# Kernel tuning notes

Hardware: AMD Instinct MI355X
Metric: run time of the kernel (lower is better)

Reference implementation:

```python
import jax, jax.numpy as jnp
import numpy as np

B, Q, D, H, CTX, W_OUT = 2048, 256, 64, 128, 5, 32


def setup_inputs() -> dict:
    key = jax.random.key(0)
    ks = jax.random.split(key, 20)
    s = 0.05
    p = lambda k, shape: jax.random.normal(k, shape, dtype=jnp.float32) * s
    return {
        "x_in": jax.random.normal(ks[0], (B, Q, D), dtype=jnp.float32),
        "w_out": W_OUT,
        "conv_w": p(ks[1], (H, 3 * D, CTX)),
        "conv_b": p(ks[2], (H,)),
        "fc1_w": p(ks[3], (H, H)),
        "fc1_b": p(ks[4], (H,)),
        "fc2_w": p(ks[5], (D, H)),
        "fc2_b": p(ks[6], (D,)),
        "rot1_w": p(ks[7], (H, D)),
        "rot1_b": p(ks[8], (H,)),
        "rot2_w": p(ks[9], (2, H)),
        "rot2_b": p(ks[10], (2,)),
        "gru_wih": p(ks[11], (3 * H, D)),
        "gru_whh": p(ks[12], (3 * H, H)),
        "gru_bih": p(ks[13], (3 * H,)),
        "gru_bhh": p(ks[14], (3 * H,)),
        "out_w": p(ks[15], (D, H)),
        "out_b": p(ks[16], (D,)),
    }


def reference(x_in, w_out, conv_w, conv_b, fc1_w, fc1_b, fc2_w, fc2_b,
              rot1_w, rot1_b, rot2_w, rot2_b, gru_wih, gru_whh,
              gru_bih, gru_bhh, out_w, out_b):
    b, q, d = x_in.shape
    h_dim = fc1_w.shape[0]
    ctx = conv_w.shape[2]
    m = d // 2
    pi = np.float32(np.pi)

    def kalman_step(carry, y_t):
        x_post, y_prev, buf = carry
        # rotation params from posterior state
        rp = jnp.maximum(x_post @ rot1_w.T + rot1_b, 0.0) @ rot2_w.T + rot2_b
        rho = jax.nn.sigmoid(rp[:, 0:1]) * 1.5
        phi = jnp.tanh(rp[:, 1:2]) * pi
        # complex polar rotation: (a+ib) * rho*e^{i phi}
        a, bb = x_post[:, :m], x_post[:, m:]
        c = rho * jnp.cos(phi)
        s = rho * jnp.sin(phi)
        x_pri = jnp.concatenate([a * c - bb * s, a * s + bb * c], axis=1)
        innov = y_t - x_pri
        diff = y_t - y_prev
        feat = jnp.concatenate([innov, x_post, diff], axis=1)  # (B, 3D)
        # roll context buffer, append newest features
        buf = jnp.concatenate([buf[:, :, 1:], feat[:, :, None]], axis=2)
        # Conv1d(kernel=context, pad=0) over a context-length buffer == full contraction
        t = jnp.einsum('hck,bck->bh', conv_w, buf) + conv_b
        t = jnp.maximum(t, 0.0)
        t = jnp.maximum(t @ fc1_w.T + fc1_b, 0.0)
        K = jax.nn.sigmoid(t @ fc2_w.T + fc2_b)  # (B, D)
        x_post_new = x_pri + K * innov
        return (x_post_new, y_t, buf), None

    init = (jnp.zeros((b, d), x_in.dtype),
            x_in[:, 0, :],
            jnp.zeros((b, 3 * d, ctx), x_in.dtype))
    (x_post, _, _), _ = jax.lax.scan(kalman_step, init, jnp.swapaxes(x_in, 0, 1))

    def gru_step(carry, _):
        h, curr = carry
        gi = curr @ gru_wih.T + gru_bih
        gh = h @ gru_whh.T + gru_bhh
        i_r, i_z, i_n = jnp.split(gi, 3, axis=1)
        h_r, h_z, h_n = jnp.split(gh, 3, axis=1)
        r = jax.nn.sigmoid(i_r + h_r)
        z = jax.nn.sigmoid(i_z + h_z)
        n = jnp.tanh(i_n + r * h_n)
        h_new = (1.0 - z) * n + z * h
        curr_new = curr + (h_new @ out_w.T + out_b)
        return (h_new, curr_new), curr_new

    (_, _), preds = jax.lax.scan(
        gru_step, (jnp.zeros((b, h_dim), x_in.dtype), x_post), None, length=w_out)
    return jnp.swapaxes(preds, 0, 1)  # (B, w_out, D)
```

## Files before the change

kernel.cpp:

```cpp
#include <hip/hip_runtime.h>

#define QLEN 256
#define DDIM 64
#define WOUT 32

typedef __bf16 b8v __attribute__((ext_vector_type(8)));
typedef float f4v __attribute__((ext_vector_type(4)));

__device__ __forceinline__ f4v MFMA(b8v a, b8v b, f4v c) {
  return __builtin_amdgcn_mfma_f32_16x16x32_bf16(a, b, c, 0, 0, 0);
}
__device__ __forceinline__ float sigmoidf_(float x) { return 1.0f/(1.0f+__expf(-x)); }
__device__ __forceinline__ float tanhf_(float x)    { return 1.0f - 2.0f/(__expf(2.0f*x)+1.0f); }
__device__ __forceinline__ b8v lda(const __bf16* p, const __bf16* zp, bool pr) {
  return *(const b8v*)(pr ? p : zp);
}

__global__ __launch_bounds__(512, 2)
void k_kalman(const float* __restrict__ x_in,
              const float* __restrict__ conv_w, const float* __restrict__ conv_b,
              const float* __restrict__ fc1_w,  const float* __restrict__ fc1_b,
              const float* __restrict__ fc2_w,  const float* __restrict__ fc2_b,
              const float* __restrict__ rot1_w, const float* __restrict__ rot1_b,
              const float* __restrict__ rot2_w, const float* __restrict__ rot2_b,
              float* __restrict__ out)
{
  __shared__ __align__(16) __bf16 SMB[11872];
  __shared__ __align__(16) float  SMF[1536];
  const int tid = threadIdx.x;
  const int w  = tid >> 6;
  const int l  = tid & 63;
  const int lr = l & 15;
  const int lg = l >> 4;
  const int wg = blockIdx.x;
  const bool pr8 = (lr < 8);

  __bf16* XPB  = SMB;
  __bf16* T1   = SMB + 576;
  __bf16* TC   = SMB + 1664;
  __bf16* T2   = SMB + 2752;
  __bf16* FEAT = SMB + 3840;
  const __bf16* ZP = SMB + 11840;
  float*  XPF  = SMF;
  float*  XPRI = SMF + 512;
  float*  INV  = SMF + 1024;

  for (int i = tid; i < 11872; i += 512) SMB[i] = (__bf16)0.0f;
  for (int i = tid; i < 1536;  i += 512) SMF[i] = 0.0f;

  const int hcol = 16*w + lr;

  b8v r1B[2], f1B[4], f2B[4], cvB[30];
  #pragma unroll
  for (int q = 0; q < 2; ++q)
    #pragma unroll
    for (int j = 0; j < 8; ++j)
      r1B[q][j] = (__bf16)rot1_w[hcol*64 + q*32 + lg*8 + j];
  #pragma unroll
  for (int q = 0; q < 4; ++q)
    #pragma unroll
    for (int j = 0; j < 8; ++j)
      f1B[q][j] = (__bf16)fc1_w[hcol*128 + q*32 + lg*8 + j];
  {
    const int h2 = (w < 4) ? hcol : 0;
    #pragma unroll
    for (int q = 0; q < 4; ++q)
      #pragma unroll
      for (int j = 0; j < 8; ++j)
        f2B[q][j] = (__bf16)fc2_w[h2*128 + q*32 + lg*8 + j];
  }
  #pragma unroll
  for (int c = 0; c < 30; ++c) {
    const int L = c/6, q = c%6;
    #pragma unroll
    for (int j = 0; j < 8; ++j)
      cvB[c][j] = (__bf16)conv_w[hcol*960 + (q*32 + lg*8 + j)*5 + (4-L)];
  }

  const float b_r1 = rot1_b[hcol];
  const float b_f1 = fc1_b[hcol];
  const float b_f2 = fc2_b[(w < 4) ? hcol : 0];
  const float bc   = conv_b[hcol];
  const float r2w00 = rot2_w[l],       r2w01 = rot2_w[64 + l];
  const float r2w10 = rot2_w[128 + l], r2w11 = rot2_w[192 + l];
  const float rb0 = rot2_b[0], rb1 = rot2_b[1];
  const float PI_F = 3.14159274f;

  const float* xptr = x_in + ((long)(wg*8 + w)*QLEN)*DDIM + l;
  float y_cur = xptr[0];
  float y_prv = y_cur;
  int slot = 0;

  __syncthreads();

  for (int t = 0; t < QLEN; ++t) {
    {
      b8v a0 = lda(&XPB[lr*72      + lg*8], ZP, pr8);
      b8v a1 = lda(&XPB[lr*72 + 32 + lg*8], ZP, pr8);
      f4v C = {};
      C = MFMA(a0, r1B[0], C);
      C = MFMA(a1, r1B[1], C);
      if (lg < 2) {
        #pragma unroll
        for (int r = 0; r < 4; ++r) {
          float v = C[r] + b_r1; v = v > 0.f ? v : 0.f;
          T1[(lg*4+r)*136 + hcol] = (__bf16)v;
        }
      }
    }
    __syncthreads();

    float y_nxt = (t+1 < QLEN) ? xptr[(t+1)*DDIM] : y_cur;
    f4v Ca = {}, Cb = {};
    {
      const __bf16* fb1 = FEAT + ((slot-1+5)%5)*1600 + lr*200 + lg*8;
      const __bf16* fb2 = FEAT + ((slot-2+5)%5)*1600 + lr*200 + lg*8;
      const __bf16* fb3 = FEAT + ((slot-3+5)%5)*1600 + lr*200 + lg*8;
      const __bf16* fb4 = FEAT + ((slot-4+5)%5)*1600 + lr*200 + lg*8;
      #pragma unroll
      for (int c = 6; c < 30; ++c) {
        const int L = c/6, q = c%6;
        const __bf16* fb = (L==1) ? fb1 : (L==2) ? fb2 : (L==3) ? fb3 : fb4;
        b8v a = lda(&fb[q*32], ZP, pr8);
        if (c & 1) Cb = MFMA(a, cvB[c], Cb); else Ca = MFMA(a, cvB[c], Ca);
      }
    }
    {
      float t1a = (float)T1[w*136 + l];
      float t1b = (float)T1[w*136 + 64 + l];
      float acc0 = t1a*r2w00 + t1b*r2w01;
      float acc1 = t1a*r2w10 + t1b*r2w11;
      #pragma unroll
      for (int m = 1; m < 64; m <<= 1) {
        acc0 += __shfl_xor(acc0, m, 64);
        acc1 += __shfl_xor(acc1, m, 64);
      }
      float rho = 1.5f * sigmoidf_(acc0 + rb0);
      float phi = PI_F * tanhf_(acc1 + rb1);
      float cc = rho * __cosf(phi);
      float ss = rho * __sinf(phi);
      float lo32 = XPF[w*64 + (l & 31)];
      float hi32 = XPF[w*64 + (l & 31) + 32];
      float xpri = (l < 32) ? (lo32*cc - hi32*ss) : (lo32*ss + hi32*cc);
      float innov = y_cur - xpri;
      float diff  = y_cur - y_prv;
      __bf16* fr = FEAT + slot*1600 + w*200;
      fr[l]       = (__bf16)innov;
      fr[128 + l] = (__bf16)diff;
      XPRI[w*64 + l] = xpri;
      INV [w*64 + l] = innov;
    }
    __syncthreads();

    {
      const __bf16* fb0 = FEAT + slot*1600 + lr*200 + lg*8;
      #pragma unroll
      for (int c = 0; c < 6; ++c) {
        b8v a = lda(&fb0[c*32], ZP, pr8);
        if (c & 1) Cb = MFMA(a, cvB[c], Cb); else Ca = MFMA(a, cvB[c], Ca);
      }
      if (lg < 2) {
        #pragma unroll
        for (int r = 0; r < 4; ++r) {
          float v = Ca[r] + Cb[r] + bc; v = v > 0.f ? v : 0.f;
          TC[(lg*4+r)*136 + hcol] = (__bf16)v;
        }
      }
    }
    __syncthreads();

    {
      f4v D0 = {}, D1 = {};
      #pragma unroll
      for (int q = 0; q < 4; ++q) {
        b8v a = lda(&TC[lr*136 + q*32 + lg*8], ZP, pr8);
        if (q & 1) D1 = MFMA(a, f1B[q], D1); else D0 = MFMA(a, f1B[q], D0);
      }
      if (lg < 2) {
        #pragma unroll
        for (int r = 0; r < 4; ++r) {
          float v = D0[r] + D1[r] + b_f1; v = v > 0.f ? v : 0.f;
          T2[(lg*4+r)*136 + hcol] = (__bf16)v;
        }
      }
    }
    __syncthreads();

    const int slot_next = (slot == 4) ? 0 : slot + 1;
    if (w < 4) {
      f4v D0 = {}, D1 = {};
      #pragma unroll
      for (int q = 0; q < 4; ++q) {
        b8v a = lda(&T2[lr*136 + q*32 + lg*8], ZP, pr8);
        if (q & 1) D1 = MFMA(a, f2B[q], D1); else D0 = MFMA(a, f2B[q], D0);
      }
      if (lg < 2) {
        #pragma unroll
        for (int r = 0; r < 4; ++r) {
          int e = lg*4 + r;
          float K = sigmoidf_(D0[r] + D1[r] + b_f2);
          float xn = XPRI[e*64 + hcol] + K * INV[e*64 + hcol];
          XPF[e*64 + hcol] = xn;
          XPB[e*72 + hcol] = (__bf16)xn;
          FEAT[slot_next*1600 + e*200 + 64 + hcol] = (__bf16)xn;
        }
      }
    }
    __syncthreads();

    y_prv = y_cur; y_cur = y_nxt;
    slot = slot_next;
  }

  out[((long)(wg*8 + w)*WOUT)*DDIM + l] = XPF[w*64 + l];
}

__global__ __launch_bounds__(512, 2)
void k_gru(const float* __restrict__ gru_wih, const float* __restrict__ gru_whh,
           const float* __restrict__ gru_bih, const float* __restrict__ gru_bhh,
           const float* __restrict__ out_w,   const float* __restrict__ out_b,
           float* __restrict__ out)
{
  __shared__ __align__(16) __bf16 CUR[16*72];
  __shared__ __align__(16) __bf16 HB [16*136];
  const int tid = threadIdx.x;
  const int w  = tid >> 6, l = tid & 63, lr = l & 15, lg = l >> 4;
  const int g = blockIdx.x;

  for (int i = tid; i < 16*136; i += 512) HB[i] = (__bf16)0.f;
  for (int i = tid; i < 16*72; i += 512) CUR[i] = (__bf16)0.f;
  __syncthreads();
  for (int i = tid; i < 8*64; i += 512) {
    int e = i >> 6, d = i & 63;
    CUR[e*72 + d] = (__bf16)out[((long)(g*8 + e)*WOUT)*DDIM + d];
  }

  b8v fih[3][2], fhh[3][4], fo[4];
  #pragma unroll
  for (int n3 = 0; n3 < 3; ++n3) {
    int row = 16*(w + 8*n3) + lr;
    #pragma unroll
    for (int q = 0; q < 2; ++q)
      #pragma unroll
      for (int j = 0; j < 8; ++j)
        fih[n3][q][j] = (__bf16)gru_wih[row*64 + q*32 + lg*8 + j];
    #pragma unroll
    for (int q = 0; q < 4; ++q)
      #pragma unroll
      for (int j = 0; j < 8; ++j)
        fhh[n3][q][j] = (__bf16)gru_whh[row*128 + q*32 + lg*8 + j];
  }
  {
    int row = 16*(w & 3) + lr;
    #pragma unroll
    for (int q = 0; q < 4; ++q)
      #pragma unroll
      for (int j = 0; j < 8; ++j)
        fo[q][j] = (__bf16)out_w[row*128 + q*32 + lg*8 + j];
  }
  const int jh = 16*w + lr;
  const float b_ir = gru_bih[jh], b_iz = gru_bih[128+jh], b_in = gru_bih[256+jh];
  const float b_hr = gru_bhh[jh], b_hz = gru_bhh[128+jh], b_hn = gru_bhh[256+jh];
  const float b_o  = out_b[16*(w & 3) + lr];
  const int dcol = 16*(w & 3) + lr;
  __syncthreads();

  for (int s = 0; s < WOUT; ++s) {
    f4v cI[3] = {}, cH[3] = {};
    #pragma unroll
    for (int q = 0; q < 2; ++q) {
      b8v a = *(const b8v*)&CUR[lr*72 + q*32 + lg*8];
      #pragma unroll
      for (int n3 = 0; n3 < 3; ++n3) cI[n3] = MFMA(a, fih[n3][q], cI[n3]);
    }
    #pragma unroll
    for (int q = 0; q < 4; ++q) {
      b8v a = *(const b8v*)&HB[lr*136 + q*32 + lg*8];
      #pragma unroll
      for (int n3 = 0; n3 < 3; ++n3) cH[n3] = MFMA(a, fhh[n3][q], cH[n3]);
    }
    __syncthreads();

    #pragma unroll
    for (int r = 0; r < 4; ++r) {
      int e = lg*4 + r;
      float ir = cI[0][r] + b_ir, iz = cI[1][r] + b_iz, in_ = cI[2][r] + b_in;
      float hr = cH[0][r] + b_hr, hz = cH[1][r] + b_hz, hn  = cH[2][r] + b_hn;
      float rr = sigmoidf_(ir + hr);
      float zz = sigmoidf_(iz + hz);
      float nn = tanhf_(in_ + rr*hn);
      float hold = (float)HB[e*136 + jh];
      float hnew = (1.f - zz)*nn + zz*hold;
      HB[e*136 + jh] = (__bf16)hnew;
    }
    __syncthreads();

    if (w < 4) {
      f4v C0 = {};
      #pragma unroll
      for (int q = 0; q < 4; ++q) {
        b8v a = *(const b8v*)&HB[lr*136 + q*32 + lg*8];
        C0 = MFMA(a, fo[q], C0);
      }
      #pragma unroll
      for (int r = 0; r < 4; ++r) {
        int e = lg*4 + r;
        float cn = (float)CUR[e*72 + dcol] + C0[r] + b_o;
        CUR[e*72 + dcol] = (__bf16)cn;
        if (e < 8)
          out[(((long)(g*8 + e))*WOUT + s)*DDIM + dcol] = cn;
      }
    }
    __syncthreads();
  }
}

extern "C" void kernel_launch(void* const* d_in, const int* in_sizes, int n_in,
                              void* d_out, int out_size, void* d_ws, size_t ws_size,
                              hipStream_t stream) {
  (void)in_sizes; (void)n_in; (void)d_ws; (void)ws_size; (void)out_size;
  const float* x_in   = (const float*)d_in[0];
  const float* conv_w = (const float*)d_in[2];
  const float* conv_b = (const float*)d_in[3];
  const float* fc1_w  = (const float*)d_in[4];
  const float* fc1_b  = (const float*)d_in[5];
  const float* fc2_w  = (const float*)d_in[6];
  const float* fc2_b  = (const float*)d_in[7];
  const float* rot1_w = (const float*)d_in[8];
  const float* rot1_b = (const float*)d_in[9];
  const float* rot2_w = (const float*)d_in[10];
  const float* rot2_b = (const float*)d_in[11];
  const float* gwih   = (const float*)d_in[12];
  const float* gwhh   = (const float*)d_in[13];
  const float* gbih   = (const float*)d_in[14];
  const float* gbhh   = (const float*)d_in[15];
  const float* ow     = (const float*)d_in[16];
  const float* ob     = (const float*)d_in[17];
  float* out = (float*)d_out;

  k_kalman<<<256, 512, 0, stream>>>(x_in, conv_w, conv_b, fc1_w, fc1_b,
                                    fc2_w, fc2_b, rot1_w, rot1_b,
                                    rot2_w, rot2_b, out);
  k_gru<<<256, 512, 0, stream>>>(gwih, gwhh, gbih, gbhh, ow, ob, out);
}
```

Measured before the change: 692.6 us.

## Split conv contraction across wave pairs with LDS partial-sum reduction

Each wave now computes two conv output tiles over half of the 30 K-chunks instead of one tile over all 30. Waves 0-3 and 4-7 split the chunks and reduce their partial sums through a new shared buffer, which costs one extra barrier per step. The current-step chunks are ordered last in the split, so less work waits behind the feature-write barrier. Per-lane shared-memory pointers are hoisted out of the loop in place of per-load select logic, and three accumulator pairs give more independent MFMA chains.

```diff
diff --git a/kernel.cpp b/kernel.cpp
--- a/kernel.cpp
+++ b/kernel.cpp
@@ -12,9 +12,6 @@
 }
 __device__ __forceinline__ float sigmoidf_(float x) { return 1.0f/(1.0f+__expf(-x)); }
 __device__ __forceinline__ float tanhf_(float x)    { return 1.0f - 2.0f/(__expf(2.0f*x)+1.0f); }
-__device__ __forceinline__ b8v lda(const __bf16* p, const __bf16* zp, bool pr) {
-  return *(const b8v*)(pr ? p : zp);
-}
 
 __global__ __launch_bounds__(512, 2)
 void k_kalman(const float* __restrict__ x_in,
@@ -25,14 +22,15 @@
               const float* __restrict__ rot2_w, const float* __restrict__ rot2_b,
               float* __restrict__ out)
 {
-  __shared__ __align__(16) __bf16 SMB[11872];
-  __shared__ __align__(16) float  SMF[1536];
+  __shared__ __align__(16) __bf16 SMB[12064];
+  __shared__ __align__(16) float  SMF[3584];
   const int tid = threadIdx.x;
   const int w  = tid >> 6;
   const int l  = tid & 63;
   const int lr = l & 15;
   const int lg = l >> 4;
   const int wg = blockIdx.x;
+  const bool lo  = (w < 4);
   const bool pr8 = (lr < 8);
 
   __bf16* XPB  = SMB;
@@ -40,17 +38,22 @@
   __bf16* TC   = SMB + 1664;
   __bf16* T2   = SMB + 2752;
   __bf16* FEAT = SMB + 3840;
-  const __bf16* ZP = SMB + 11840;
+  __bf16* ZROW = SMB + 11856;
   float*  XPF  = SMF;
   float*  XPRI = SMF + 512;
   float*  INV  = SMF + 1024;
-
-  for (int i = tid; i < 11872; i += 512) SMB[i] = (__bf16)0.0f;
-  for (int i = tid; i < 1536;  i += 512) SMF[i] = 0.0f;
+  float*  PART = SMF + 1536;
+
+  for (int i = tid; i < 12064; i += 512) SMB[i] = (__bf16)0.0f;
+  for (int i = tid; i < 3584;  i += 512) SMF[i] = 0.0f;
 
   const int hcol = 16*w + lr;
-
-  b8v r1B[2], f1B[4], f2B[4], cvB[30];
+  const int t0   = 2*(w & 3);
+
+  constexpr int CH_LO[15] = {2, 6,7,8, 12,13,14, 18,19,20, 24,25,26, 0,1};
+  constexpr int CH_HI[15] = {3, 9,10,11, 15,16,17, 21,22,23, 27,28,29, 4,5};
+
+  b8v r1B[2], f1B[4], f2B[4], cvB[15][2];
   #pragma unroll
   for (int q = 0; q < 2; ++q)
     #pragma unroll
@@ -62,7 +65,7 @@
     for (int j = 0; j < 8; ++j)
       f1B[q][j] = (__bf16)fc1_w[hcol*128 + q*32 + lg*8 + j];
   {
-    const int h2 = (w < 4) ? hcol : 0;
+    const int h2 = lo ? hcol : 0;
     #pragma unroll
     for (int q = 0; q < 4; ++q)
       #pragma unroll
@@ -70,22 +73,33 @@
         f2B[q][j] = (__bf16)fc2_w[h2*128 + q*32 + lg*8 + j];
   }
   #pragma unroll
-  for (int c = 0; c < 30; ++c) {
+  for (int i = 0; i < 15; ++i) {
+    const int c = lo ? CH_LO[i] : CH_HI[i];
     const int L = c/6, q = c%6;
     #pragma unroll
-    for (int j = 0; j < 8; ++j)
-      cvB[c][j] = (__bf16)conv_w[hcol*960 + (q*32 + lg*8 + j)*5 + (4-L)];
+    for (int ti = 0; ti < 2; ++ti)
+      #pragma unroll
+      for (int j = 0; j < 8; ++j)
+        cvB[i][ti][j] =
+          (__bf16)conv_w[((t0+ti)*16 + lr)*960 + (q*32 + lg*8 + j)*5 + (4-L)];
   }
 
   const float b_r1 = rot1_b[hcol];
   const float b_f1 = fc1_b[hcol];
-  const float b_f2 = fc2_b[(w < 4) ? hcol : 0];
-  const float bc   = conv_b[hcol];
+  const float b_f2 = fc2_b[lo ? hcol : 0];
+  const float bc0  = conv_b[t0*16 + lr];
+  const float bc1  = conv_b[(t0+1)*16 + lr];
   const float r2w00 = rot2_w[l],       r2w01 = rot2_w[64 + l];
   const float r2w10 = rot2_w[128 + l], r2w11 = rot2_w[192 + l];
   const float rb0 = rot2_b[0], rb1 = rot2_b[1];
   const float PI_F = 3.14159274f;
 
+  const __bf16* zb    = ZROW + lg*8;
+  const __bf16* xpb_p = pr8 ? (XPB + lr*72  + lg*8) : zb;
+  const __bf16* tc_p  = pr8 ? (TC  + lr*136 + lg*8) : zb;
+  const __bf16* t2_p  = pr8 ? (T2  + lr*136 + lg*8) : zb;
+  const __bf16* featb = FEAT + lr*200 + lg*8;
+
   const float* xptr = x_in + ((long)(wg*8 + w)*QLEN)*DDIM + l;
   float y_cur = xptr[0];
   float y_prv = y_cur;
@@ -95,8 +109,8 @@
 
   for (int t = 0; t < QLEN; ++t) {
     {
-      b8v a0 = lda(&XPB[lr*72      + lg*8], ZP, pr8);
-      b8v a1 = lda(&XPB[lr*72 + 32 + lg*8], ZP, pr8);
+      b8v a0 = *(const b8v*)(xpb_p);
+      b8v a1 = *(const b8v*)(xpb_p + 32);
       f4v C = {};
       C = MFMA(a0, r1B[0], C);
       C = MFMA(a1, r1B[1], C);
@@ -111,18 +125,23 @@
     __syncthreads();
 
     float y_nxt = (t+1 < QLEN) ? xptr[(t+1)*DDIM] : y_cur;
-    f4v Ca = {}, Cb = {};
-    {
-      const __bf16* fb1 = FEAT + ((slot-1+5)%5)*1600 + lr*200 + lg*8;
-      const __bf16* fb2 = FEAT + ((slot-2+5)%5)*1600 + lr*200 + lg*8;
-      const __bf16* fb3 = FEAT + ((slot-3+5)%5)*1600 + lr*200 + lg*8;
-      const __bf16* fb4 = FEAT + ((slot-4+5)%5)*1600 + lr*200 + lg*8;
-      #pragma unroll
-      for (int c = 6; c < 30; ++c) {
+    const __bf16* fbp[5];
+    #pragma unroll
+    for (int L = 0; L < 5; ++L) {
+      int s5 = slot - L; if (s5 < 0) s5 += 5;
+      fbp[L] = pr8 ? (featb + s5*1600) : zb;
+    }
+    f4v P0 = {}, P1 = {}, P2 = {}, Q0 = {}, Q1 = {}, Q2 = {};
+    {
+      #pragma unroll
+      for (int i = 0; i < 13; ++i) {
+        const int c = lo ? CH_LO[i] : CH_HI[i];
         const int L = c/6, q = c%6;
-        const __bf16* fb = (L==1) ? fb1 : (L==2) ? fb2 : (L==3) ? fb3 : fb4;
-        b8v a = lda(&fb[q*32], ZP, pr8);
-        if (c & 1) Cb = MFMA(a, cvB[c], Cb); else Ca = MFMA(a, cvB[c], Ca);
+        b8v a = *(const b8v*)&fbp[L][q*32];
+        const int s3 = i % 3;
+        if      (s3 == 0) { P0 = MFMA(a, cvB[i][0], P0); Q0 = MFMA(a, cvB[i][1], Q0); }
+        else if (s3 == 1) { P1 = MFMA(a, cvB[i][0], P1); Q1 = MFMA(a, cvB[i][1], Q1); }
+        else              { P2 = MFMA(a, cvB[i][0], P2); Q2 = MFMA(a, cvB[i][1], Q2); }
       }
     }
     {
@@ -153,17 +172,34 @@
     __syncthreads();
 
     {
-      const __bf16* fb0 = FEAT + slot*1600 + lr*200 + lg*8;
-      #pragma unroll
-      for (int c = 0; c < 6; ++c) {
-        b8v a = lda(&fb0[c*32], ZP, pr8);
-        if (c & 1) Cb = MFMA(a, cvB[c], Cb); else Ca = MFMA(a, cvB[c], Ca);
-      }
+      const __bf16* fb0 = pr8 ? (featb + slot*1600) : zb;
+      #pragma unroll
+      for (int i = 13; i < 15; ++i) {
+        const int q = (lo ? CH_LO[i] : CH_HI[i]) % 6;
+        b8v a = *(const b8v*)&fb0[q*32];
+        if (i == 13) { P0 = MFMA(a, cvB[i][0], P0); Q0 = MFMA(a, cvB[i][1], Q0); }
+        else         { P1 = MFMA(a, cvB[i][0], P1); Q1 = MFMA(a, cvB[i][1], Q1); }
+      }
+      if (!lo) {
+        f4v s0, s1;
+        #pragma unroll
+        for (int r = 0; r < 4; ++r) { s0[r] = P0[r]+P1[r]+P2[r]; s1[r] = Q0[r]+Q1[r]+Q2[r]; }
+        *(f4v*)&PART[(t0*16 + lr)*16 + lg*4]     = s0;
+        *(f4v*)&PART[((t0+1)*16 + lr)*16 + lg*4] = s1;
+      }
+    }
+    __syncthreads();
+
+    if (lo) {
+      f4v p0 = *(const f4v*)&PART[(t0*16 + lr)*16 + lg*4];
+      f4v p1 = *(const f4v*)&PART[((t0+1)*16 + lr)*16 + lg*4];
       if (lg < 2) {
         #pragma unroll
         for (int r = 0; r < 4; ++r) {
-          float v = Ca[r] + Cb[r] + bc; v = v > 0.f ? v : 0.f;
-          TC[(lg*4+r)*136 + hcol] = (__bf16)v;
+          float v0 = P0[r]+P1[r]+P2[r] + p0[r] + bc0; v0 = v0 > 0.f ? v0 : 0.f;
+          float v1 = Q0[r]+Q1[r]+Q2[r] + p1[r] + bc1; v1 = v1 > 0.f ? v1 : 0.f;
+          TC[(lg*4+r)*136 + t0*16 + lr]     = (__bf16)v0;
+          TC[(lg*4+r)*136 + (t0+1)*16 + lr] = (__bf16)v1;
         }
       }
     }
@@ -173,7 +209,7 @@
       f4v D0 = {}, D1 = {};
       #pragma unroll
       for (int q = 0; q < 4; ++q) {
-        b8v a = lda(&TC[lr*136 + q*32 + lg*8], ZP, pr8);
+        b8v a = *(const b8v*)(tc_p + q*32);
         if (q & 1) D1 = MFMA(a, f1B[q], D1); else D0 = MFMA(a, f1B[q], D0);
       }
       if (lg < 2) {
@@ -187,11 +223,11 @@
     __syncthreads();
 
     const int slot_next = (slot == 4) ? 0 : slot + 1;
-    if (w < 4) {
+    if (lo) {
       f4v D0 = {}, D1 = {};
       #pragma unroll
       for (int q = 0; q < 4; ++q) {
-        b8v a = lda(&T2[lr*136 + q*32 + lg*8], ZP, pr8);
+        b8v a = *(const b8v*)(t2_p + q*32);
         if (q & 1) D1 = MFMA(a, f2B[q], D1); else D0 = MFMA(a, f2B[q], D0);
       }
       if (lg < 2) {
```

New measurement: 1.374 ms. 98.3% more time.

## Carry conv partial sums across steps and parallelize rotation reduction

Applied to the files above, without the earlier changes.

Each feature frame's contribution to the conv is now accumulated once and carried forward in registers (U/V accumulators), so each step issues its conv MFMAs as soon as a frame is available. The history-frame MFMAs are spread over phases that were otherwise idle (alongside fc1 and fc2), taking them off the critical path. The rotation-head reduction now uses 16-lane shuffles plus a small shared partial-sum table instead of a bf16 T1 round-trip followed by a full 64-lane reduction. The predicated loads that fell back to a zero pad are dropped, and the layout of rows 8-15 relies on zero-initialized shared memory. The cost is more accumulator registers and a tighter dependency on that zero padding.

```diff
diff --git a/kernel.cpp b/kernel.cpp
--- a/kernel.cpp
+++ b/kernel.cpp
@@ -12,9 +12,6 @@
 }
 __device__ __forceinline__ float sigmoidf_(float x) { return 1.0f/(1.0f+__expf(-x)); }
 __device__ __forceinline__ float tanhf_(float x)    { return 1.0f - 2.0f/(__expf(2.0f*x)+1.0f); }
-__device__ __forceinline__ b8v lda(const __bf16* p, const __bf16* zp, bool pr) {
-  return *(const b8v*)(pr ? p : zp);
-}
 
 __global__ __launch_bounds__(512, 2)
 void k_kalman(const float* __restrict__ x_in,
@@ -25,28 +22,26 @@
               const float* __restrict__ rot2_w, const float* __restrict__ rot2_b,
               float* __restrict__ out)
 {
-  __shared__ __align__(16) __bf16 SMB[11872];
-  __shared__ __align__(16) float  SMF[1536];
+  __shared__ __align__(16) __bf16 SMB[12352];
+  __shared__ __align__(16) float  SMF[1792];
   const int tid = threadIdx.x;
   const int w  = tid >> 6;
   const int l  = tid & 63;
   const int lr = l & 15;
   const int lg = l >> 4;
   const int wg = blockIdx.x;
-  const bool pr8 = (lr < 8);
 
   __bf16* XPB  = SMB;
-  __bf16* T1   = SMB + 576;
-  __bf16* TC   = SMB + 1664;
-  __bf16* T2   = SMB + 2752;
-  __bf16* FEAT = SMB + 3840;
-  const __bf16* ZP = SMB + 11840;
+  __bf16* TC   = SMB + 576;
+  __bf16* T2   = SMB + 1664;
+  __bf16* FEAT = SMB + 2752;
   float*  XPF  = SMF;
   float*  XPRI = SMF + 512;
   float*  INV  = SMF + 1024;
-
-  for (int i = tid; i < 11872; i += 512) SMB[i] = (__bf16)0.0f;
-  for (int i = tid; i < 1536;  i += 512) SMF[i] = 0.0f;
+  float*  PR   = SMF + 1536;
+
+  for (int i = tid; i < 12352; i += 512) SMB[i] = (__bf16)0.0f;
+  for (int i = tid; i < 1792;  i += 512) SMF[i] = 0.0f;
 
   const int hcol = 16*w + lr;
 
@@ -81,8 +76,8 @@
   const float b_f1 = fc1_b[hcol];
   const float b_f2 = fc2_b[(w < 4) ? hcol : 0];
   const float bc   = conv_b[hcol];
-  const float r2w00 = rot2_w[l],       r2w01 = rot2_w[64 + l];
-  const float r2w10 = rot2_w[128 + l], r2w11 = rot2_w[192 + l];
+  const float w2c0 = rot2_w[hcol];
+  const float w2c1 = rot2_w[128 + hcol];
   const float rb0 = rot2_b[0], rb1 = rot2_b[1];
   const float PI_F = 3.14159274f;
 
@@ -91,52 +86,60 @@
   float y_prv = y_cur;
   int slot = 0;
 
+  f4v U0 = {}, U1 = {}, U2 = {}, V0 = {}, V1 = {}, V2 = {};
+
   __syncthreads();
 
   for (int t = 0; t < QLEN; ++t) {
-    {
-      b8v a0 = lda(&XPB[lr*72      + lg*8], ZP, pr8);
-      b8v a1 = lda(&XPB[lr*72 + 32 + lg*8], ZP, pr8);
+    int m1 = slot - 1; if (m1 < 0) m1 += 5;
+    int m2 = slot - 2; if (m2 < 0) m2 += 5;
+    int m3 = slot - 3; if (m3 < 0) m3 += 5;
+    const int slot_next = (slot == 4) ? 0 : slot + 1;
+
+    {
+      const __bf16* fx = FEAT + slot*1600 + lr*200 + lg*8;
+      b8v ax2 = *(const b8v*)&fx[2*32];
+      b8v ax3 = *(const b8v*)&fx[3*32];
+      U0 = MFMA(ax2, cvB[2], U0);
+      U1 = MFMA(ax3, cvB[3], U1);
+      b8v a0 = *(const b8v*)&XPB[lr*72      + lg*8];
+      b8v a1 = *(const b8v*)&XPB[lr*72 + 32 + lg*8];
       f4v C = {};
       C = MFMA(a0, r1B[0], C);
       C = MFMA(a1, r1B[1], C);
-      if (lg < 2) {
+      float p0[4], p1[4];
+      #pragma unroll
+      for (int r = 0; r < 4; ++r) {
+        float v = C[r] + b_r1; v = v > 0.f ? v : 0.f;
+        p0[r] = v * w2c0;
+        p1[r] = v * w2c1;
+      }
+      #pragma unroll
+      for (int m = 1; m < 16; m <<= 1) {
         #pragma unroll
         for (int r = 0; r < 4; ++r) {
-          float v = C[r] + b_r1; v = v > 0.f ? v : 0.f;
-          T1[(lg*4+r)*136 + hcol] = (__bf16)v;
+          p0[r] += __shfl_xor(p0[r], m, 64);
+          p1[r] += __shfl_xor(p1[r], m, 64);
+        }
+      }
+      if (lr == 0) {
+        #pragma unroll
+        for (int r = 0; r < 4; ++r) {
+          PR[(lg*4+r)*16 + 2*w]     = p0[r];
+          PR[(lg*4+r)*16 + 2*w + 1] = p1[r];
         }
       }
     }
     __syncthreads();
 
     float y_nxt = (t+1 < QLEN) ? xptr[(t+1)*DDIM] : y_cur;
-    f4v Ca = {}, Cb = {};
-    {
-      const __bf16* fb1 = FEAT + ((slot-1+5)%5)*1600 + lr*200 + lg*8;
-      const __bf16* fb2 = FEAT + ((slot-2+5)%5)*1600 + lr*200 + lg*8;
-      const __bf16* fb3 = FEAT + ((slot-3+5)%5)*1600 + lr*200 + lg*8;
-      const __bf16* fb4 = FEAT + ((slot-4+5)%5)*1600 + lr*200 + lg*8;
-      #pragma unroll
-      for (int c = 6; c < 30; ++c) {
-        const int L = c/6, q = c%6;
-        const __bf16* fb = (L==1) ? fb1 : (L==2) ? fb2 : (L==3) ? fb3 : fb4;
-        b8v a = lda(&fb[q*32], ZP, pr8);
-        if (c & 1) Cb = MFMA(a, cvB[c], Cb); else Ca = MFMA(a, cvB[c], Ca);
-      }
-    }
-    {
-      float t1a = (float)T1[w*136 + l];
-      float t1b = (float)T1[w*136 + 64 + l];
-      float acc0 = t1a*r2w00 + t1b*r2w01;
-      float acc1 = t1a*r2w10 + t1b*r2w11;
-      #pragma unroll
-      for (int m = 1; m < 64; m <<= 1) {
-        acc0 += __shfl_xor(acc0, m, 64);
-        acc1 += __shfl_xor(acc1, m, 64);
-      }
-      float rho = 1.5f * sigmoidf_(acc0 + rb0);
-      float phi = PI_F * tanhf_(acc1 + rb1);
+    {
+      f4v s = *(const f4v*)&PR[w*16];
+      s += *(const f4v*)&PR[w*16 + 4];
+      s += *(const f4v*)&PR[w*16 + 8];
+      s += *(const f4v*)&PR[w*16 + 12];
+      float rho = 1.5f * sigmoidf_(s[0] + s[2] + rb0);
+      float phi = PI_F * tanhf_(s[1] + s[3] + rb1);
       float cc = rho * __cosf(phi);
       float ss = rho * __sinf(phi);
       float lo32 = XPF[w*64 + (l & 31)];
@@ -153,16 +156,27 @@
     __syncthreads();
 
     {
-      const __bf16* fb0 = FEAT + slot*1600 + lr*200 + lg*8;
-      #pragma unroll
-      for (int c = 0; c < 6; ++c) {
-        b8v a = lda(&fb0[c*32], ZP, pr8);
-        if (c & 1) Cb = MFMA(a, cvB[c], Cb); else Ca = MFMA(a, cvB[c], Ca);
-      }
+      const __bf16* f0 = FEAT + slot*1600 + lr*200 + lg*8;
+      b8v aq0 = *(const b8v*)&f0[0*32];
+      b8v aq1 = *(const b8v*)&f0[1*32];
+      b8v aq2 = *(const b8v*)&f0[2*32];
+      b8v aq3 = *(const b8v*)&f0[3*32];
+      b8v aq4 = *(const b8v*)&f0[4*32];
+      b8v aq5 = *(const b8v*)&f0[5*32];
+      U2 = MFMA(aq0, cvB[0], U2);
+      U0 = MFMA(aq1, cvB[1], U0);
+      U1 = MFMA(aq4, cvB[4], U1);
+      U2 = MFMA(aq5, cvB[5], U2);
+      V0 = MFMA(aq0, cvB[6],  V0);
+      V1 = MFMA(aq1, cvB[7],  V1);
+      V2 = MFMA(aq2, cvB[8],  V2);
+      V0 = MFMA(aq3, cvB[9],  V0);
+      V1 = MFMA(aq4, cvB[10], V1);
+      V2 = MFMA(aq5, cvB[11], V2);
       if (lg < 2) {
         #pragma unroll
         for (int r = 0; r < 4; ++r) {
-          float v = Ca[r] + Cb[r] + bc; v = v > 0.f ? v : 0.f;
+          float v = U0[r] + U1[r] + U2[r] + bc; v = v > 0.f ? v : 0.f;
           TC[(lg*4+r)*136 + hcol] = (__bf16)v;
         }
       }
@@ -171,10 +185,28 @@
 
     {
       f4v D0 = {}, D1 = {};
+      const __bf16* tcp = TC + lr*136 + lg*8;
       #pragma unroll
       for (int q = 0; q < 4; ++q) {
-        b8v a = lda(&TC[lr*136 + q*32 + lg*8], ZP, pr8);
+        b8v a = *(const b8v*)&tcp[q*32];
         if (q & 1) D1 = MFMA(a, f1B[q], D1); else D0 = MFMA(a, f1B[q], D0);
+      }
+      const __bf16* fl2 = FEAT + m1*1600 + lr*200 + lg*8;
+      const __bf16* fl3 = FEAT + m2*1600 + lr*200 + lg*8;
+      {
+        b8v a;
+        a = *(const b8v*)&fl2[0*32];  V0 = MFMA(a, cvB[12], V0);
+        a = *(const b8v*)&fl2[1*32];  V1 = MFMA(a, cvB[13], V1);
+        a = *(const b8v*)&fl2[2*32];  V2 = MFMA(a, cvB[14], V2);
+        a = *(const b8v*)&fl2[3*32];  V0 = MFMA(a, cvB[15], V0);
+        a = *(const b8v*)&fl2[4*32];  V1 = MFMA(a, cvB[16], V1);
+        a = *(const b8v*)&fl2[5*32];  V2 = MFMA(a, cvB[17], V2);
+        a = *(const b8v*)&fl3[0*32];  V0 = MFMA(a, cvB[18], V0);
+        a = *(const b8v*)&fl3[1*32];  V1 = MFMA(a, cvB[19], V1);
+        a = *(const b8v*)&fl3[2*32];  V2 = MFMA(a, cvB[20], V2);
+        a = *(const b8v*)&fl3[3*32];  V0 = MFMA(a, cvB[21], V0);
+        a = *(const b8v*)&fl3[4*32];  V1 = MFMA(a, cvB[22], V1);
+        a = *(const b8v*)&fl3[5*32];  V2 = MFMA(a, cvB[23], V2);
       }
       if (lg < 2) {
         #pragma unroll
@@ -186,27 +218,40 @@
     }
     __syncthreads();
 
-    const int slot_next = (slot == 4) ? 0 : slot + 1;
-    if (w < 4) {
-      f4v D0 = {}, D1 = {};
-      #pragma unroll
-      for (int q = 0; q < 4; ++q) {
-        b8v a = lda(&T2[lr*136 + q*32 + lg*8], ZP, pr8);
-        if (q & 1) D1 = MFMA(a, f2B[q], D1); else D0 = MFMA(a, f2B[q], D0);
-      }
-      if (lg < 2) {
-        #pragma unroll
-        for (int r = 0; r < 4; ++r) {
-          int e = lg*4 + r;
-          float K = sigmoidf_(D0[r] + D1[r] + b_f2);
-          float xn = XPRI[e*64 + hcol] + K * INV[e*64 + hcol];
-          XPF[e*64 + hcol] = xn;
-          XPB[e*72 + hcol] = (__bf16)xn;
-          FEAT[slot_next*1600 + e*200 + 64 + hcol] = (__bf16)xn;
-        }
-      }
-    }
-    __syncthreads();
+    {
+      const __bf16* fl4 = FEAT + m3*1600 + lr*200 + lg*8;
+      b8v a;
+      a = *(const b8v*)&fl4[0*32];  V0 = MFMA(a, cvB[24], V0);
+      a = *(const b8v*)&fl4[1*32];  V1 = MFMA(a, cvB[25], V1);
+      a = *(const b8v*)&fl4[2*32];  V2 = MFMA(a, cvB[26], V2);
+      a = *(const b8v*)&fl4[3*32];  V0 = MFMA(a, cvB[27], V0);
+      a = *(const b8v*)&fl4[4*32];  V1 = MFMA(a, cvB[28], V1);
+      a = *(const b8v*)&fl4[5*32];  V2 = MFMA(a, cvB[29], V2);
+      if (w < 4) {
+        f4v D0 = {}, D1 = {};
+        const __bf16* t2p = T2 + lr*136 + lg*8;
+        #pragma unroll
+        for (int q = 0; q < 4; ++q) {
+          b8v b = *(const b8v*)&t2p[q*32];
+          if (q & 1) D1 = MFMA(b, f2B[q], D1); else D0 = MFMA(b, f2B[q], D0);
+        }
+        if (lg < 2) {
+          #pragma unroll
+          for (int r = 0; r < 4; ++r) {
+            int e = lg*4 + r;
+            float K = sigmoidf_(D0[r] + D1[r] + b_f2);
+            float xn = XPRI[e*64 + hcol] + K * INV[e*64 + hcol];
+            XPF[e*64 + hcol] = xn;
+            XPB[e*72 + hcol] = (__bf16)xn;
+            FEAT[slot_next*1600 + e*200 + 64 + hcol] = (__bf16)xn;
+          }
+        }
+      }
+    }
+    __syncthreads();
+
+    U0 = V0; U1 = V1; U2 = V2;
+    V0 = (f4v){}; V1 = (f4v){}; V2 = (f4v){};
 
     y_prv = y_cur; y_cur = y_nxt;
     slot = slot_next;
```

Result: slower. 803.7 us (+16.0%).
